# Kernel optimization log

Hardware: AMD Instinct MI355X
Metric: run time of the kernel (lower is better)

The kernel has to match this reference:

```python
import jax, jax.numpy as jnp
import numpy as np

KNOW, ITEM, D, L, LAT, B, S = 1024, 20000, 128, 2, 256, 256, 200
NTOT = ITEM + KNOW
E1, E2 = 32768, 160000


def graph_layer(h, W, a, src, dst, n):
    # GAT-style: gather src/dst, edge MLP, segment softmax over dst, weighted scatter-sum
    z = h @ W                                              # [N, D]
    e = jax.nn.leaky_relu((jnp.concatenate([z[src], z[dst]], axis=-1) @ a)[:, 0])  # [E]
    m = jax.ops.segment_max(e, dst, num_segments=n)
    m = jnp.where(jnp.isfinite(m), m, 0.0)                 # nodes with no in-edges
    w = jnp.exp(e - m[dst])                                # [E]
    den = jax.ops.segment_sum(w, dst, num_segments=n)      # [N]
    num = jax.ops.segment_sum(w[:, None] * z[src], dst, num_segments=n)  # [N, D]
    return jnp.where(den[:, None] > 0, num / jnp.maximum(den, 1e-12)[:, None], 0.0)


def setup_inputs() -> dict:
    key = jax.random.key(0)
    ks = jax.random.split(key, 32)
    p = lambda i, shp: jax.random.normal(ks[i], shp, dtype=jnp.float32) * 0.05
    inp = {
        'p_rec': jax.random.randint(ks[0], (B, S), 0, ITEM),
        'p_target': jax.random.randint(ks[1], (B,), 0, S),
        'a_rec': jax.random.randint(ks[2], (B, S), 0, 3),
        'kn_rec': jax.random.uniform(ks[3], (B, S, KNOW), dtype=jnp.float32),
        'kn_num': jnp.ones((B, S), dtype=jnp.float32),
        'src1': jax.random.randint(ks[4], (E1,), 0, KNOW),
        'dst1': jax.random.randint(ks[5], (E1,), 0, KNOW),
        'src2': jax.random.randint(ks[6], (E2,), 0, NTOT),
        'dst2': jax.random.randint(ks[7], (E2,), 0, NTOT),
        'src3': jax.random.randint(ks[8], (E2,), 0, NTOT),
        'dst3': jax.random.randint(ks[9], (E2,), 0, NTOT),
        'kn_table': p(10, (KNOW, D)),
        'exer_table': p(11, (ITEM, D)),
        'ans_table': p(12, (3, D)),
        'gW': p(13, (L, 3, D, D)),
        'gA': p(14, (L, 3, 2 * D, 1)),
        'raW1': p(15, (L, D, D)),
        'raB1': jnp.zeros((L, D), jnp.float32),
        'raW2': p(16, (L, D, 1)),
        'actW1': p(17, (3 * D, LAT)),
        'actB1': jnp.zeros((LAT,), jnp.float32),
        'actW2': p(18, (LAT, ITEM)),
        'actB2': jnp.zeros((ITEM,), jnp.float32),
        'vW1': p(19, (3, 3 * D, LAT)),
        'vB1': jnp.zeros((3, LAT), jnp.float32),
        'vW2': p(20, (3, LAT, 1)),
        'vB2': jnp.zeros((3, 1), jnp.float32),
    }
    return inp


def reference(p_rec, p_target, a_rec, kn_rec, kn_num, src1, dst1, src2, dst2, src3, dst3,
              kn_table, exer_table, ans_table, gW, gA, raW1, raB1, raW2,
              actW1, actB1, actW2, actB2, vW1, vB1, vW2, vB2):
    kn, ex = kn_table, exer_table
    for l in range(L):  # GraphEncoder: stacked Fusion blocks (distinct params)
        k_dir = graph_layer(kn, gW[l, 0], gA[l, 0], src1, dst1, KNOW)
        ek = jnp.concatenate([ex, kn], axis=0)             # [NTOT, D]
        kfe = graph_layer(ek, gW[l, 1], gA[l, 1], src2, dst2, NTOT)
        efk = graph_layer(ek, gW[l, 2], gA[l, 2], src3, dst3, NTOT)
        A_, B_ = k_dir, kfe[ITEM:]
        ra = lambda x: jnp.tanh(x @ raW1[l] + raB1[l]) @ raW2[l]  # [KNOW, 1]
        s = jax.nn.softmax(jnp.concatenate([ra(A_), ra(B_)], axis=1), axis=1)
        kn = s[:, :1] * A_ + s[:, 1:2] * B_
        ex = efk[:ITEM]
    # hidden_layer
    be = ex[p_rec]                                         # [B, S, D]
    ba = ans_table[a_rec]                                  # [B, S, D]
    bk = jnp.einsum('bsk,kd->bsd', kn_rec, kn) / kn_num[..., None]
    item = jnp.concatenate([be, ba, bk], axis=-1)          # [B, S, 3D]
    m = (jnp.arange(S)[None, :] < (p_target + 1)[:, None]).astype(item.dtype)
    h = (item * m[..., None]).sum(axis=1) / m.sum(axis=1, keepdims=True)  # [B, 3D]
    logits = jnp.tanh(h @ actW1 + actB1) @ actW2 + actB2   # [B, ITEM]
    vh = jnp.tanh(jnp.einsum('bd,kdl->kbl', h, vW1) + vB1[:, None, :])
    vals = jnp.einsum('kbl,klo->kbo', vh, vW2) + vB2[:, None, :]  # [3, B, 1]
    return logits, vals[0], vals[1], vals[2]
```

## Files before the change

### kernel.cpp

```cpp
#include <hip/hip_runtime.h>

#define D 128
#define KNOW 1024
#define ITEM 20000
#define NTOT (ITEM + KNOW)
#define LAYERS 2
#define LAT 256
#define BB 256
#define SS 200
#define H3 (3 * D)
#define CH 4
#define ZROWS 64
#define NBK (KNOW / ZROWS)
#define NBN ((NTOT + ZROWS - 1) / ZROWS)
#define NZT (NBK + 2 * NBN)
#define NAGGU (KNOW / 4 + ITEM / 4)
#define NKROW (BB * CH)
#define XPITCH 68
#define NLOGB ((ITEM + 255) / 256)
#define NLV (NLOGB * (BB / 32))
#define NVB ((3 * BB + 3) / 4)

__global__ __launch_bounds__(256) void zdv_ker(
    const float* __restrict__ Xe, const float* __restrict__ Xk,
    const float* __restrict__ gW, const float* __restrict__ gA, int layer,
    float* __restrict__ z1, float* __restrict__ z2, float* __restrict__ z3,
    float* __restrict__ ds1, float* __restrict__ dd1,
    float* __restrict__ ds2, float* __restrict__ dd2,
    float* __restrict__ ds3, float* __restrict__ dd3)
{
    __shared__ __align__(16) float xT[D * XPITCH];
    int bid = blockIdx.x;
    int g, row0, nmax;
    if (bid < NBK)            { g = 0; row0 = bid * ZROWS;                nmax = KNOW; }
    else if (bid < NBK + NBN) { g = 1; row0 = (bid - NBK) * ZROWS;        nmax = NTOT; }
    else                      { g = 2; row0 = (bid - NBK - NBN) * ZROWS;  nmax = NTOT; }
    const float* W = gW + (size_t)(layer * 3 + g) * D * D;
    const float* A = gA + (size_t)(layer * 3 + g) * 2 * D;
    float* Z  = (g == 0) ? z1  : (g == 1 ? z2  : z3);
    float* DS = (g == 0) ? ds1 : (g == 1 ? ds2 : ds3);
    float* DD = (g == 0) ? dd1 : (g == 1 ? dd2 : dd3);

    int tid = threadIdx.x;
#pragma unroll
    for (int i = 0; i < 8; ++i) {
        int flat = tid + i * 256;
        int row  = flat >> 5;
        int f4   = flat & 31;
        int grow = row0 + row;
        float4 v = make_float4(0.f, 0.f, 0.f, 0.f);
        if (grow < nmax) {
            const float* src = (g == 0) ? (Xk + (size_t)grow * D)
                             : (grow < ITEM ? Xe + (size_t)grow * D
                                            : Xk + (size_t)(grow - ITEM) * D);
            v = *(const float4*)(src + f4 * 4);
        }
        int slot = row ^ ((f4 & 7) << 2);
        int kk = f4 * 4;
        xT[(kk + 0) * XPITCH + slot] = v.x;
        xT[(kk + 1) * XPITCH + slot] = v.y;
        xT[(kk + 2) * XPITCH + slot] = v.z;
        xT[(kk + 3) * XPITCH + slot] = v.w;
    }
    __syncthreads();

    int cg_ = tid & 31;
    int rg = tid >> 5;
    int c0 = cg_ * 4;
    int r0a = rg * 8, r0b = rg * 8 + 4;

    float acc[8][4];
#pragma unroll
    for (int r = 0; r < 8; ++r)
#pragma unroll
        for (int c = 0; c < 4; ++c) acc[r][c] = 0.f;

#pragma unroll 4
    for (int k = 0; k < D; ++k) {
        float4 wv = *(const float4*)(W + (size_t)k * D + c0);
        int xc = ((k >> 2) & 7) << 2;
        float4 xa = *(const float4*)&xT[k * XPITCH + (r0a ^ xc)];
        float4 xb = *(const float4*)&xT[k * XPITCH + (r0b ^ xc)];
        acc[0][0] = fmaf(xa.x, wv.x, acc[0][0]); acc[0][1] = fmaf(xa.x, wv.y, acc[0][1]);
        acc[0][2] = fmaf(xa.x, wv.z, acc[0][2]); acc[0][3] = fmaf(xa.x, wv.w, acc[0][3]);
        acc[1][0] = fmaf(xa.y, wv.x, acc[1][0]); acc[1][1] = fmaf(xa.y, wv.y, acc[1][1]);
        acc[1][2] = fmaf(xa.y, wv.z, acc[1][2]); acc[1][3] = fmaf(xa.y, wv.w, acc[1][3]);
        acc[2][0] = fmaf(xa.z, wv.x, acc[2][0]); acc[2][1] = fmaf(xa.z, wv.y, acc[2][1]);
        acc[2][2] = fmaf(xa.z, wv.z, acc[2][2]); acc[2][3] = fmaf(xa.z, wv.w, acc[2][3]);
        acc[3][0] = fmaf(xa.w, wv.x, acc[3][0]); acc[3][1] = fmaf(xa.w, wv.y, acc[3][1]);
        acc[3][2] = fmaf(xa.w, wv.z, acc[3][2]); acc[3][3] = fmaf(xa.w, wv.w, acc[3][3]);
        acc[4][0] = fmaf(xb.x, wv.x, acc[4][0]); acc[4][1] = fmaf(xb.x, wv.y, acc[4][1]);
        acc[4][2] = fmaf(xb.x, wv.z, acc[4][2]); acc[4][3] = fmaf(xb.x, wv.w, acc[4][3]);
        acc[5][0] = fmaf(xb.y, wv.x, acc[5][0]); acc[5][1] = fmaf(xb.y, wv.y, acc[5][1]);
        acc[5][2] = fmaf(xb.y, wv.z, acc[5][2]); acc[5][3] = fmaf(xb.y, wv.w, acc[5][3]);
        acc[6][0] = fmaf(xb.z, wv.x, acc[6][0]); acc[6][1] = fmaf(xb.z, wv.y, acc[6][1]);
        acc[6][2] = fmaf(xb.z, wv.z, acc[6][2]); acc[6][3] = fmaf(xb.z, wv.w, acc[6][3]);
        acc[7][0] = fmaf(xb.w, wv.x, acc[7][0]); acc[7][1] = fmaf(xb.w, wv.y, acc[7][1]);
        acc[7][2] = fmaf(xb.w, wv.z, acc[7][2]); acc[7][3] = fmaf(xb.w, wv.w, acc[7][3]);
    }

#pragma unroll
    for (int r = 0; r < 8; ++r) {
        int grow = row0 + ((r < 4) ? (r0a + r) : (r0b + r - 4));
        if (grow < nmax) {
            float4 v = make_float4(acc[r][0], acc[r][1], acc[r][2], acc[r][3]);
            *(float4*)(Z + (size_t)grow * D + c0) = v;
        }
    }

    float4 as = *(const float4*)(A + c0);
    float4 ad = *(const float4*)(A + D + c0);
    float ps[8], pd[8];
#pragma unroll
    for (int r = 0; r < 8; ++r) {
        ps[r] = acc[r][0] * as.x + acc[r][1] * as.y + acc[r][2] * as.z + acc[r][3] * as.w;
        pd[r] = acc[r][0] * ad.x + acc[r][1] * ad.y + acc[r][2] * ad.z + acc[r][3] * ad.w;
    }
#pragma unroll
    for (int m = 16; m; m >>= 1) {
#pragma unroll
        for (int r = 0; r < 8; ++r) {
            ps[r] += __shfl_xor(ps[r], m, 64);
            pd[r] += __shfl_xor(pd[r], m, 64);
        }
    }
    if (cg_ == 0) {
#pragma unroll
        for (int r = 0; r < 8; ++r) {
            int grow = row0 + ((r < 4) ? (r0a + r) : (r0b + r - 4));
            if (grow < nmax) { DS[grow] = ps[r]; DD[grow] = pd[r]; }
        }
    }
}

__global__ void hist3(const int* __restrict__ d1, const int* __restrict__ d2, const int* __restrict__ d3,
                      int E1, int E2, int* __restrict__ c1, int* __restrict__ c2, int* __restrict__ c3) {
    int i = blockIdx.x * blockDim.x + threadIdx.x;
    if (i < E1) atomicAdd(&c1[d1[i]], 1);
    else if (i < E1 + E2) { int d = d2[i - E1]; if (d >= ITEM) atomicAdd(&c2[d - ITEM], 1); }
    else if (i < E1 + 2 * E2) { int d = d3[i - E1 - E2]; if (d < ITEM) atomicAdd(&c3[d], 1); }
}

__global__ __launch_bounds__(1024) void exscan3(int* __restrict__ c1, int* __restrict__ o1,
                                                int* __restrict__ c2, int* __restrict__ o2,
                                                int* __restrict__ c3, int* __restrict__ o3) {
    int g = blockIdx.x;
    int* cnt = (g == 0) ? c1 : (g == 1 ? c2 : c3);
    int* off = (g == 0) ? o1 : (g == 1 ? o2 : o3);
    int n = (g == 2) ? ITEM : KNOW;
    int tid = threadIdx.x, lane = tid & 63, wid = tid >> 6;
    int L = (n + 1023) >> 10;
    int i0 = tid * L;
    int sum = 0;
    for (int q = 0; q < L; ++q) {
        int i = i0 + q;
        if (i < n) sum += cnt[i];
    }
    int x = sum;
#pragma unroll
    for (int d = 1; d < 64; d <<= 1) { int t = __shfl_up(x, d, 64); if (lane >= d) x += t; }
    __shared__ int ws[16];
    if (lane == 63) ws[wid] = x;
    __syncthreads();
    if (wid == 0) {
        int w = (lane < 16) ? ws[lane] : 0;
#pragma unroll
        for (int d = 1; d < 16; d <<= 1) { int t = __shfl_up(w, d, 64); if (lane >= d) w += t; }
        if (lane < 16) ws[lane] = w;
    }
    __syncthreads();
    int run = x - sum + ((wid > 0) ? ws[wid - 1] : 0);
    if (tid == 0) off[0] = 0;
    for (int q = 0; q < L; ++q) {
        int i = i0 + q;
        if (i < n) {
            int v = cnt[i];
            cnt[i] = run;
            run += v;
            off[i + 1] = run;
        }
    }
}

__global__ void scatter3(const int* __restrict__ s1, const int* __restrict__ d1,
                         const int* __restrict__ s2, const int* __restrict__ d2,
                         const int* __restrict__ s3, const int* __restrict__ d3,
                         int E1, int E2, int* __restrict__ cur1, int* __restrict__ cur2, int* __restrict__ cur3,
                         int* __restrict__ e1, int* __restrict__ e2, int* __restrict__ e3) {
    int i = blockIdx.x * blockDim.x + threadIdx.x;
    if (i < E1) { int p = atomicAdd(&cur1[d1[i]], 1); e1[p] = s1[i]; }
    else if (i < E1 + E2) { int j = i - E1; int d = d2[j]; if (d >= ITEM) { int p = atomicAdd(&cur2[d - ITEM], 1); e2[p] = s2[j]; } }
    else if (i < E1 + 2 * E2) { int j = i - E1 - E2; int d = d3[j]; if (d < ITEM) { int p = atomicAdd(&cur3[d], 1); e3[p] = s3[j]; } }
}

__device__ __forceinline__ void agg_row(const float* __restrict__ Z, const float* __restrict__ dsrc,
                                        float dd, const int* __restrict__ es, int e0, int e1,
                                        int lane, float* __restrict__ acc) {
#pragma unroll
    for (int q = 0; q < 8; ++q) acc[q] = 0.f;
    if (e1 <= e0) return;
    float mx = -3.4e38f;
    for (int e = e0 + lane; e < e1; e += 64) {
        float t = dsrc[es[e]] + dd;
        t = (t > 0.f) ? t : 0.01f * t;
        mx = fmaxf(mx, t);
    }
#pragma unroll
    for (int o = 32; o; o >>= 1) mx = fmaxf(mx, __shfl_xor(mx, o, 64));
    int eg = lane >> 4, cs = lane & 15;
    float den = 0.f;
    for (int e = e0 + eg; e < e1; e += 4) {
        int s = es[e];
        float t = dsrc[s] + dd;
        t = (t > 0.f) ? t : 0.01f * t;
        float w = __expf(t - mx);
        den += w;
        const float4* zr = (const float4*)(Z + (size_t)s * D + cs * 8);
        float4 za = zr[0], zb = zr[1];
        acc[0] = fmaf(w, za.x, acc[0]); acc[1] = fmaf(w, za.y, acc[1]);
        acc[2] = fmaf(w, za.z, acc[2]); acc[3] = fmaf(w, za.w, acc[3]);
        acc[4] = fmaf(w, zb.x, acc[4]); acc[5] = fmaf(w, zb.y, acc[5]);
        acc[6] = fmaf(w, zb.z, acc[6]); acc[7] = fmaf(w, zb.w, acc[7]);
    }
#pragma unroll
    for (int m = 16; m <= 32; m <<= 1) {
        den += __shfl_xor(den, m, 64);
#pragma unroll
        for (int q = 0; q < 8; ++q) acc[q] += __shfl_xor(acc[q], m, 64);
    }
    float inv = 1.f / fmaxf(den, 1e-12f);
#pragma unroll
    for (int q = 0; q < 8; ++q) acc[q] *= inv;
}

__global__ __launch_bounds__(256) void agg3c(
    const float* __restrict__ z1, const float* __restrict__ z2, const float* __restrict__ z3,
    const float* __restrict__ ds1, const float* __restrict__ dd1,
    const float* __restrict__ ds2, const float* __restrict__ dd2,
    const float* __restrict__ ds3, const float* __restrict__ dd3,
    const int* __restrict__ off1, const int* __restrict__ es1,
    const int* __restrict__ off2, const int* __restrict__ es2,
    const int* __restrict__ off3, const int* __restrict__ es3,
    const float* __restrict__ raW1L, const float* __restrict__ raB1L,
    const float* __restrict__ raW2L, float* __restrict__ buf,
    const float* __restrict__ kn_rec, const float* __restrict__ kn_num,
    const int* __restrict__ p_target, float* __restrict__ krowP)
{
    int wv = threadIdx.x >> 6, lane = threadIdx.x & 63;
    int eg = lane >> 4, cs = lane & 15;
    int u = blockIdx.x;
    if (u < KNOW / 4) {
        __shared__ float ABs[4][2][D];
        int i = u * 4 + wv;
        float accA[8], accB[8];
        agg_row(z1, ds1, dd1[i], es1, off1[i], off1[i + 1], lane, accA);
        agg_row(z2, ds2, dd2[ITEM + i], es2, off2[i], off2[i + 1], lane, accB);
        if (eg == 0) {
            *(float4*)&ABs[wv][0][cs * 8]     = make_float4(accA[0], accA[1], accA[2], accA[3]);
            *(float4*)&ABs[wv][0][cs * 8 + 4] = make_float4(accA[4], accA[5], accA[6], accA[7]);
            *(float4*)&ABs[wv][1][cs * 8]     = make_float4(accB[0], accB[1], accB[2], accB[3]);
            *(float4*)&ABs[wv][1][cs * 8 + 4] = make_float4(accB[4], accB[5], accB[6], accB[7]);
        }
        __syncthreads();
        int j0 = lane * 2;
        float b0 = raB1L[j0], b1 = raB1L[j0 + 1];
        float aA0 = b0, aA1 = b1, aB0 = b0, aB1 = b1;
#pragma unroll 4
        for (int k = 0; k < D; ++k) {
            float av = ABs[wv][0][k], bv = ABs[wv][1][k];
            float2 w = *(const float2*)(raW1L + (size_t)k * D + j0);
            aA0 = fmaf(av, w.x, aA0); aA1 = fmaf(av, w.y, aA1);
            aB0 = fmaf(bv, w.x, aB0); aB1 = fmaf(bv, w.y, aB1);
        }
        float2 w2 = *(const float2*)(raW2L + j0);
        float pA = tanhf(aA0) * w2.x + tanhf(aA1) * w2.y;
        float pB = tanhf(aB0) * w2.x + tanhf(aB1) * w2.y;
#pragma unroll
        for (int o = 32; o; o >>= 1) { pA += __shfl_xor(pA, o, 64); pB += __shfl_xor(pB, o, 64); }
        float mx2 = fmaxf(pA, pB);
        float eA = __expf(pA - mx2), eB = __expf(pB - mx2);
        float s = 1.f / (eA + eB);
        float sA = eA * s, sB = eB * s;
        float2 Av = *(float2*)&ABs[wv][0][j0];
        float2 Bv = *(float2*)&ABs[wv][1][j0];
        *(float2*)(buf + (size_t)(ITEM + i) * D + j0) =
            make_float2(sA * Av.x + sB * Bv.x, sA * Av.y + sB * Bv.y);
    } else if (u < NAGGU) {
        int row = (u - KNOW / 4) * 4 + wv;
        if (row < ITEM) {
            float acc[8];
            agg_row(z3, ds3, dd3[row], es3, off3[row], off3[row + 1], lane, acc);
            if (eg == 0) {
                *(float4*)(buf + (size_t)row * D + cs * 8)     = make_float4(acc[0], acc[1], acc[2], acc[3]);
                *(float4*)(buf + (size_t)row * D + cs * 8 + 4) = make_float4(acc[4], acc[5], acc[6], acc[7]);
            }
        }
    } else {
        int uk = u - NAGGU;
        int b = uk & (BB - 1), ch = uk >> 8;
        int cnt = p_target[b] + 1;
        int per = (SS + CH - 1) / CH;
        int s0 = ch * per, s1 = s0 + per;
        if (s1 > cnt) s1 = cnt;
        int k0 = threadIdx.x * 4;
        float4 a = make_float4(0.f, 0.f, 0.f, 0.f);
        for (int s = s0; s < s1; ++s) {
            float inv = 1.f / kn_num[b * SS + s];
            float4 v = *(const float4*)(kn_rec + ((size_t)b * SS + s) * KNOW + k0);
            a.x += v.x * inv; a.y += v.y * inv; a.z += v.z * inv; a.w += v.w * inv;
        }
        *(float4*)(krowP + ((size_t)ch * BB + b) * KNOW + k0) = a;
    }
}

__global__ __launch_bounds__(512) void hker(const float* __restrict__ ex, const float* __restrict__ ans_table,
                                            const int* __restrict__ p_rec, const int* __restrict__ a_rec,
                                            const int* __restrict__ p_target, const float* __restrict__ krowP,
                                            const float* __restrict__ kn, float* __restrict__ h) {
    int b = blockIdx.x;
    int j = threadIdx.x & 127, sg = threadIdx.x >> 7;
    int cnt = p_target[b] + 1;
    __shared__ int pidx[SS], aidx[SS];
    __shared__ float kr[KNOW];
    __shared__ float red[4][3][128];
    for (int i = threadIdx.x; i < cnt; i += 512) { pidx[i] = p_rec[b * SS + i]; aidx[i] = a_rec[b * SS + i]; }
    for (int i = threadIdx.x; i < KNOW; i += 512) {
        float s = 0.f;
#pragma unroll
        for (int c = 0; c < CH; ++c) s += krowP[((size_t)c * BB + b) * KNOW + i];
        kr[i] = s;
    }
    __syncthreads();
    float accE = 0.f, accA = 0.f;
    for (int s = sg; s < cnt; s += 4) {
        accE += ex[(size_t)pidx[s] * D + j];
        accA += ans_table[aidx[s] * D + j];
    }
    float accK = 0.f;
    for (int k = sg * 256; k < sg * 256 + 256; ++k) accK += kr[k] * kn[(size_t)k * D + j];
    red[sg][0][j] = accE; red[sg][1][j] = accA; red[sg][2][j] = accK;
    __syncthreads();
    if (sg == 0) {
        float inv = 1.f / (float)cnt;
        float e = (red[0][0][j] + red[1][0][j] + red[2][0][j] + red[3][0][j]) * inv;
        float a = (red[0][1][j] + red[1][1][j] + red[2][1][j] + red[3][1][j]) * inv;
        float kv = (red[0][2][j] + red[1][2][j] + red[2][2][j] + red[3][2][j]) * inv;
        h[b * H3 + j] = e;
        h[b * H3 + D + j] = a;
        h[b * H3 + 2 * D + j] = kv;
    }
}

__global__ __launch_bounds__(256) void hidden_gemm(const float* __restrict__ h,
                                                   const float* __restrict__ actW1, const float* __restrict__ actB1,
                                                   const float* __restrict__ vW1, const float* __restrict__ vB1,
                                                   float* __restrict__ hid) {
    __shared__ float hT[H3 * 17];
    int tid = threadIdx.x;
    int b0 = blockIdx.y * 16;
    for (int idx = tid; idx < 16 * H3; idx += 256) {
        int r = idx / H3, k = idx - r * H3;
        hT[k * 17 + r] = h[(size_t)(b0 + r) * H3 + k];
    }
    __syncthreads();
    int j = blockIdx.x * 64 + (tid & 63);
    int head = j >> 8, jj = j & 255;
    int rg = tid >> 6, r0 = rg * 4;
    const float* W = (head == 0) ? actW1 : (vW1 + (size_t)(head - 1) * H3 * LAT);
    float bias = (head == 0) ? actB1[jj] : vB1[(head - 1) * LAT + jj];
    float acc[4] = {bias, bias, bias, bias};
#pragma unroll 4
    for (int k = 0; k < H3; ++k) {
        float w = W[(size_t)k * LAT + jj];
        float h0 = hT[k * 17 + r0 + 0];
        float h1 = hT[k * 17 + r0 + 1];
        float h2 = hT[k * 17 + r0 + 2];
        float h3 = hT[k * 17 + r0 + 3];
        acc[0] = fmaf(h0, w, acc[0]);
        acc[1] = fmaf(h1, w, acc[1]);
        acc[2] = fmaf(h2, w, acc[2]);
        acc[3] = fmaf(h3, w, acc[3]);
    }
#pragma unroll
    for (int r = 0; r < 4; ++r)
        hid[((size_t)head * BB + (b0 + r0 + r)) * LAT + jj] = tanhf(acc[r]);
}

__global__ __launch_bounds__(256) void logitsvals(const float* __restrict__ hid,
                                                  const float* __restrict__ actW2, const float* __restrict__ actB2,
                                                  const float* __restrict__ vW2, const float* __restrict__ vB2,
                                                  float* __restrict__ out) {
    int bid = blockIdx.x;
    int tid = threadIdx.x;
    if (bid < NLV) {
        __shared__ float hT[LAT * 33];
        int ix = bid % NLOGB, iy = bid / NLOGB;
        int b0 = iy * 32;
        for (int idx = tid; idx < 32 * LAT; idx += 256) {
            int r = idx >> 8, k = idx & 255;
            hT[k * 33 + r] = hid[(size_t)(b0 + r) * LAT + k];
        }
        __syncthreads();
        int lane6 = tid & 63;
        int rg = tid >> 6, r0 = rg * 8;
        int ibase = ix * 256 + lane6;
        int icol[4], icl[4];
        float bias[4];
#pragma unroll
        for (int c = 0; c < 4; ++c) {
            icol[c] = ibase + c * 64;
            icl[c] = icol[c] < ITEM ? icol[c] : (ITEM - 1);
            bias[c] = actB2[icl[c]];
        }
        float acc[8][4];
#pragma unroll
        for (int r = 0; r < 8; ++r)
#pragma unroll
            for (int c = 0; c < 4; ++c) acc[r][c] = bias[c];
#pragma unroll 2
        for (int k = 0; k < LAT; ++k) {
            float w0 = actW2[(size_t)k * ITEM + icl[0]];
            float w1 = actW2[(size_t)k * ITEM + icl[1]];
            float w2 = actW2[(size_t)k * ITEM + icl[2]];
            float w3 = actW2[(size_t)k * ITEM + icl[3]];
            const float* hp = &hT[k * 33 + r0];
#pragma unroll
            for (int r = 0; r < 8; ++r) {
                float hv = hp[r];
                acc[r][0] = fmaf(hv, w0, acc[r][0]);
                acc[r][1] = fmaf(hv, w1, acc[r][1]);
                acc[r][2] = fmaf(hv, w2, acc[r][2]);
                acc[r][3] = fmaf(hv, w3, acc[r][3]);
            }
        }
#pragma unroll
        for (int c = 0; c < 4; ++c) {
            if (icol[c] < ITEM) {
#pragma unroll
                for (int r = 0; r < 8; ++r)
                    out[(size_t)(b0 + r0 + r) * ITEM + icol[c]] = acc[r][c];
            }
        }
    } else {
        int idx = (bid - NLV) * 4 + (tid >> 6);
        int lane = tid & 63;
        if (idx >= 3 * BB) return;
        int k = idx / BB, b = idx - k * BB;
        const float* vh = hid + ((size_t)(k + 1) * BB + b) * LAT;
        float4 a = ((const float4*)vh)[lane];
        float4 w = ((const float4*)(vW2 + k * LAT))[lane];
        float s = a.x * w.x + a.y * w.y + a.z * w.z + a.w * w.w;
#pragma unroll
        for (int o = 32; o; o >>= 1) s += __shfl_down(s, o, 64);
        if (lane == 0) out[(size_t)BB * ITEM + k * BB + b] = s + vB2[k];
    }
}

extern "C" void kernel_launch(void* const* d_in, const int* in_sizes, int n_in,
                              void* d_out, int out_size, void* d_ws, size_t ws_size,
                              hipStream_t stream) {
    const int*   p_rec      = (const int*)d_in[0];
    const int*   p_target   = (const int*)d_in[1];
    const int*   a_rec      = (const int*)d_in[2];
    const float* kn_rec     = (const float*)d_in[3];
    const float* kn_num     = (const float*)d_in[4];
    const int*   src1       = (const int*)d_in[5];
    const int*   dst1       = (const int*)d_in[6];
    const int*   src2       = (const int*)d_in[7];
    const int*   dst2       = (const int*)d_in[8];
    const int*   src3       = (const int*)d_in[9];
    const int*   dst3       = (const int*)d_in[10];
    const float* kn_table   = (const float*)d_in[11];
    const float* exer_table = (const float*)d_in[12];
    const float* ans_table  = (const float*)d_in[13];
    const float* gW         = (const float*)d_in[14];
    const float* gA         = (const float*)d_in[15];
    const float* raW1       = (const float*)d_in[16];
    const float* raB1       = (const float*)d_in[17];
    const float* raW2       = (const float*)d_in[18];
    const float* actW1      = (const float*)d_in[19];
    const float* actB1      = (const float*)d_in[20];
    const float* actW2      = (const float*)d_in[21];
    const float* actB2      = (const float*)d_in[22];
    const float* vW1        = (const float*)d_in[23];
    const float* vB1        = (const float*)d_in[24];
    const float* vW2        = (const float*)d_in[25];
    const float* vB2        = (const float*)d_in[26];
    const int E1 = in_sizes[5], E2 = in_sizes[7];

    float* base = (float*)d_ws;
    size_t o = 0;
    auto alloc = [&](size_t n) -> float* { float* p = base + o; o += (n + 3) & ~(size_t)3; return p; };
    float* buf  = alloc((size_t)NTOT * D);
    float* z1   = alloc((size_t)KNOW * D);
    float* z2   = alloc((size_t)NTOT * D);
    float* z3   = alloc((size_t)NTOT * D);
    float* ds1 = alloc(KNOW);  float* dd1 = alloc(KNOW);
    float* ds2 = alloc(NTOT);  float* dd2 = alloc(NTOT);
    float* ds3 = alloc(NTOT);  float* dd3 = alloc(NTOT);
    int* cnts = (int*)alloc(2 * KNOW + NTOT);
    int* cnt1 = cnts, *cnt2 = cnts + KNOW, *cnt3 = cnts + 2 * KNOW;
    int* off1 = (int*)alloc(KNOW + 1);
    int* off2 = (int*)alloc(KNOW + 1);
    int* off3 = (int*)alloc(ITEM + 1);
    int* es1  = (int*)alloc(E1);
    int* es2  = (int*)alloc(E2);
    int* es3  = (int*)alloc(E2);
    float* krowP = alloc((size_t)CH * BB * KNOW);
    float* hbuf  = alloc((size_t)BB * H3);
    float* hid   = alloc((size_t)4 * BB * LAT);

    hipMemsetAsync(cnts, 0, sizeof(int) * (2 * KNOW + NTOT), stream);

    int etot = E1 + 2 * E2;
    hist3<<<(etot + 255) / 256, 256, 0, stream>>>(dst1, dst2, dst3, E1, E2, cnt1, cnt2, cnt3);
    exscan3<<<3, 1024, 0, stream>>>(cnt1, off1, cnt2, off2, cnt3, off3);
    scatter3<<<(etot + 255) / 256, 256, 0, stream>>>(src1, dst1, src2, dst2, src3, dst3,
                                                     E1, E2, cnt1, cnt2, cnt3, es1, es2, es3);

    for (int l = 0; l < LAYERS; ++l) {
        const float* Xe = (l == 0) ? exer_table : buf;
        const float* Xk = (l == 0) ? kn_table : (buf + (size_t)ITEM * D);
        zdv_ker<<<NZT, 256, 0, stream>>>(Xe, Xk, gW, gA, l, z1, z2, z3,
                                         ds1, dd1, ds2, dd2, ds3, dd3);
        int nb = NAGGU + ((l == 0) ? NKROW : 0);
        agg3c<<<nb, 256, 0, stream>>>(z1, z2, z3, ds1, dd1, ds2, dd2, ds3, dd3,
                                      off1, es1, off2, es2, off3, es3,
                                      raW1 + (size_t)l * D * D, raB1 + (size_t)l * D,
                                      raW2 + (size_t)l * D, buf,
                                      kn_rec, kn_num, p_target, krowP);
    }

    hker<<<BB, 512, 0, stream>>>(buf, ans_table, p_rec, a_rec, p_target, krowP, buf + (size_t)ITEM * D, hbuf);
    hidden_gemm<<<dim3(16, 16), 256, 0, stream>>>(hbuf, actW1, actB1, vW1, vB1, hid);
    logitsvals<<<NLV + NVB, 256, 0, stream>>>(hid, actW2, actB2, vW2, vB2, (float*)d_out);
}
```

Baseline: 303.5 us.

## Fold graph-2 projection past aggregation and drop softmax max pass

Graph 2 only needs outputs for the KNOW target nodes. Its full-NTOT z=h@W is removed: the attention logits use a precomputed W·a vector applied to the raw inputs, the raw X rows are aggregated, and W is multiplied in afterwards for only the 1024 knowledge rows. Input and output buffers are double-buffered because agg3c now reads the previous layer's X. The segment-max pass in the softmax is also removed and exp is applied to unshifted logits, which saves a full edge sweep but risks overflow for large logits.

```diff
diff --git a/kernel.cpp b/kernel.cpp
--- a/kernel.cpp
+++ b/kernel.cpp
@@ -13,7 +13,7 @@
 #define ZROWS 64
 #define NBK (KNOW / ZROWS)
 #define NBN ((NTOT + ZROWS - 1) / ZROWS)
-#define NZT (NBK + 2 * NBN)
+#define NZT (NBK + NBN)
 #define NAGGU (KNOW / 4 + ITEM / 4)
 #define NKROW (BB * CH)
 #define XPITCH 68
@@ -23,8 +23,9 @@
 
 __global__ __launch_bounds__(256) void zdv_ker(
     const float* __restrict__ Xe, const float* __restrict__ Xk,
-    const float* __restrict__ gW, const float* __restrict__ gA, int layer,
-    float* __restrict__ z1, float* __restrict__ z2, float* __restrict__ z3,
+    const float* __restrict__ gW, const float* __restrict__ gA,
+    const float* __restrict__ wa2, int layer,
+    float* __restrict__ z1, float* __restrict__ z3,
     float* __restrict__ ds1, float* __restrict__ dd1,
     float* __restrict__ ds2, float* __restrict__ dd2,
     float* __restrict__ ds3, float* __restrict__ dd3)
@@ -32,14 +33,13 @@
     __shared__ __align__(16) float xT[D * XPITCH];
     int bid = blockIdx.x;
     int g, row0, nmax;
-    if (bid < NBK)            { g = 0; row0 = bid * ZROWS;                nmax = KNOW; }
-    else if (bid < NBK + NBN) { g = 1; row0 = (bid - NBK) * ZROWS;        nmax = NTOT; }
-    else                      { g = 2; row0 = (bid - NBK - NBN) * ZROWS;  nmax = NTOT; }
+    if (bid < NBK) { g = 0; row0 = bid * ZROWS;          nmax = KNOW; }
+    else           { g = 2; row0 = (bid - NBK) * ZROWS;  nmax = NTOT; }
     const float* W = gW + (size_t)(layer * 3 + g) * D * D;
     const float* A = gA + (size_t)(layer * 3 + g) * 2 * D;
-    float* Z  = (g == 0) ? z1  : (g == 1 ? z2  : z3);
-    float* DS = (g == 0) ? ds1 : (g == 1 ? ds2 : ds3);
-    float* DD = (g == 0) ? dd1 : (g == 1 ? dd2 : dd3);
+    float* Z  = (g == 0) ? z1  : z3;
+    float* DS = (g == 0) ? ds1 : ds3;
+    float* DD = (g == 0) ? dd1 : dd3;
 
     int tid = threadIdx.x;
 #pragma unroll
@@ -131,6 +131,40 @@
             if (grow < nmax) { DS[grow] = ps[r]; DD[grow] = pd[r]; }
         }
     }
+
+    if (g == 2) {
+        const float* was = wa2 + (size_t)layer * 2 * D;
+        float4 ws4 = *(const float4*)(was + c0);
+        float4 wd4 = *(const float4*)(was + D + c0);
+        int xc = ((c0 >> 2) & 7) << 2;
+        float pxs[8], pxd[8];
+#pragma unroll
+        for (int r = 0; r < 8; ++r) {
+            int rr = (r < 4) ? (r0a + r) : (r0b + r - 4);
+            int sl = rr ^ xc;
+            float x0 = xT[(c0 + 0) * XPITCH + sl];
+            float x1 = xT[(c0 + 1) * XPITCH + sl];
+            float x2 = xT[(c0 + 2) * XPITCH + sl];
+            float x3 = xT[(c0 + 3) * XPITCH + sl];
+            pxs[r] = x0 * ws4.x + x1 * ws4.y + x2 * ws4.z + x3 * ws4.w;
+            pxd[r] = x0 * wd4.x + x1 * wd4.y + x2 * wd4.z + x3 * wd4.w;
+        }
+#pragma unroll
+        for (int m = 16; m; m >>= 1) {
+#pragma unroll
+            for (int r = 0; r < 8; ++r) {
+                pxs[r] += __shfl_xor(pxs[r], m, 64);
+                pxd[r] += __shfl_xor(pxd[r], m, 64);
+            }
+        }
+        if (cg_ == 0) {
+#pragma unroll
+            for (int r = 0; r < 8; ++r) {
+                int grow = row0 + ((r < 4) ? (r0a + r) : (r0b + r - 4));
+                if (grow < nmax) { ds2[grow] = pxs[r]; dd2[grow] = pxd[r]; }
+            }
+        }
+    }
 }
 
 __global__ void hist3(const int* __restrict__ d1, const int* __restrict__ d2, const int* __restrict__ d3,
@@ -143,8 +177,24 @@
 
 __global__ __launch_bounds__(1024) void exscan3(int* __restrict__ c1, int* __restrict__ o1,
                                                 int* __restrict__ c2, int* __restrict__ o2,
-                                                int* __restrict__ c3, int* __restrict__ o3) {
+                                                int* __restrict__ c3, int* __restrict__ o3,
+                                                const float* __restrict__ gW, const float* __restrict__ gA,
+                                                float* __restrict__ wa2) {
     int g = blockIdx.x;
+    if (g == 3) {
+        int t = threadIdx.x;
+        if (t < 2 * 2 * D) {
+            int l = t >> 8, rem = t & 255;
+            int v = rem >> 7, k = rem & 127;
+            const float* Wp = gW + (size_t)(l * 3 + 1) * D * D + (size_t)k * D;
+            const float* ap = gA + (size_t)(l * 3 + 1) * 2 * D + v * D;
+            float s = 0.f;
+#pragma unroll 4
+            for (int j = 0; j < D; ++j) s = fmaf(Wp[j], ap[j], s);
+            wa2[(l * 2 + v) * D + k] = s;
+        }
+        return;
+    }
     int* cnt = (g == 0) ? c1 : (g == 1 ? c2 : c3);
     int* off = (g == 0) ? o1 : (g == 1 ? o2 : o3);
     int n = (g == 2) ? ITEM : KNOW;
@@ -199,21 +249,14 @@
 #pragma unroll
     for (int q = 0; q < 8; ++q) acc[q] = 0.f;
     if (e1 <= e0) return;
-    float mx = -3.4e38f;
-    for (int e = e0 + lane; e < e1; e += 64) {
-        float t = dsrc[es[e]] + dd;
-        t = (t > 0.f) ? t : 0.01f * t;
-        mx = fmaxf(mx, t);
-    }
-#pragma unroll
-    for (int o = 32; o; o >>= 1) mx = fmaxf(mx, __shfl_xor(mx, o, 64));
     int eg = lane >> 4, cs = lane & 15;
     float den = 0.f;
+#pragma unroll 2
     for (int e = e0 + eg; e < e1; e += 4) {
         int s = es[e];
         float t = dsrc[s] + dd;
         t = (t > 0.f) ? t : 0.01f * t;
-        float w = __expf(t - mx);
+        float w = __expf(t);
         den += w;
         const float4* zr = (const float4*)(Z + (size_t)s * D + cs * 8);
         float4 za = zr[0], zb = zr[1];
@@ -233,16 +276,53 @@
     for (int q = 0; q < 8; ++q) acc[q] *= inv;
 }
 
+__device__ __forceinline__ void agg_rowX(const float* __restrict__ Xe, const float* __restrict__ Xk,
+                                         const float* __restrict__ dsrc, float dd,
+                                         const int* __restrict__ es, int e0, int e1,
+                                         int lane, float* __restrict__ acc) {
+#pragma unroll
+    for (int q = 0; q < 8; ++q) acc[q] = 0.f;
+    if (e1 <= e0) return;
+    int eg = lane >> 4, cs = lane & 15;
+    float den = 0.f;
+#pragma unroll 2
+    for (int e = e0 + eg; e < e1; e += 4) {
+        int s = es[e];
+        float t = dsrc[s] + dd;
+        t = (t > 0.f) ? t : 0.01f * t;
+        float w = __expf(t);
+        den += w;
+        const float* xr = (s < ITEM) ? (Xe + (size_t)s * D) : (Xk + (size_t)(s - ITEM) * D);
+        const float4* zr = (const float4*)(xr + cs * 8);
+        float4 za = zr[0], zb = zr[1];
+        acc[0] = fmaf(w, za.x, acc[0]); acc[1] = fmaf(w, za.y, acc[1]);
+        acc[2] = fmaf(w, za.z, acc[2]); acc[3] = fmaf(w, za.w, acc[3]);
+        acc[4] = fmaf(w, zb.x, acc[4]); acc[5] = fmaf(w, zb.y, acc[5]);
+        acc[6] = fmaf(w, zb.z, acc[6]); acc[7] = fmaf(w, zb.w, acc[7]);
+    }
+#pragma unroll
+    for (int m = 16; m <= 32; m <<= 1) {
+        den += __shfl_xor(den, m, 64);
+#pragma unroll
+        for (int q = 0; q < 8; ++q) acc[q] += __shfl_xor(acc[q], m, 64);
+    }
+    float inv = 1.f / fmaxf(den, 1e-12f);
+#pragma unroll
+    for (int q = 0; q < 8; ++q) acc[q] *= inv;
+}
+
 __global__ __launch_bounds__(256) void agg3c(
-    const float* __restrict__ z1, const float* __restrict__ z2, const float* __restrict__ z3,
+    const float* __restrict__ Xe, const float* __restrict__ Xk,
+    const float* __restrict__ z1, const float* __restrict__ z3,
     const float* __restrict__ ds1, const float* __restrict__ dd1,
     const float* __restrict__ ds2, const float* __restrict__ dd2,
     const float* __restrict__ ds3, const float* __restrict__ dd3,
     const int* __restrict__ off1, const int* __restrict__ es1,
     const int* __restrict__ off2, const int* __restrict__ es2,
     const int* __restrict__ off3, const int* __restrict__ es3,
+    const float* __restrict__ gW1L,
     const float* __restrict__ raW1L, const float* __restrict__ raB1L,
-    const float* __restrict__ raW2L, float* __restrict__ buf,
+    const float* __restrict__ raW2L, float* __restrict__ out,
     const float* __restrict__ kn_rec, const float* __restrict__ kn_num,
     const int* __restrict__ p_target, float* __restrict__ krowP)
 {
@@ -251,10 +331,11 @@
     int u = blockIdx.x;
     if (u < KNOW / 4) {
         __shared__ float ABs[4][2][D];
+        __shared__ float Bf[4][D];
         int i = u * 4 + wv;
         float accA[8], accB[8];
         agg_row(z1, ds1, dd1[i], es1, off1[i], off1[i + 1], lane, accA);
-        agg_row(z2, ds2, dd2[ITEM + i], es2, off2[i], off2[i + 1], lane, accB);
+        agg_rowX(Xe, Xk, ds2, dd2[ITEM + i], es2, off2[i], off2[i + 1], lane, accB);
         if (eg == 0) {
             *(float4*)&ABs[wv][0][cs * 8]     = make_float4(accA[0], accA[1], accA[2], accA[3]);
             *(float4*)&ABs[wv][0][cs * 8 + 4] = make_float4(accA[4], accA[5], accA[6], accA[7]);
@@ -263,11 +344,20 @@
         }
         __syncthreads();
         int j0 = lane * 2;
+        float fB0 = 0.f, fB1 = 0.f;
+#pragma unroll 4
+        for (int k = 0; k < D; ++k) {
+            float xv = ABs[wv][1][k];
+            float2 w = *(const float2*)(gW1L + (size_t)k * D + j0);
+            fB0 = fmaf(xv, w.x, fB0); fB1 = fmaf(xv, w.y, fB1);
+        }
+        Bf[wv][j0] = fB0; Bf[wv][j0 + 1] = fB1;
+        __syncthreads();
         float b0 = raB1L[j0], b1 = raB1L[j0 + 1];
         float aA0 = b0, aA1 = b1, aB0 = b0, aB1 = b1;
 #pragma unroll 4
         for (int k = 0; k < D; ++k) {
-            float av = ABs[wv][0][k], bv = ABs[wv][1][k];
+            float av = ABs[wv][0][k], bv = Bf[wv][k];
             float2 w = *(const float2*)(raW1L + (size_t)k * D + j0);
             aA0 = fmaf(av, w.x, aA0); aA1 = fmaf(av, w.y, aA1);
             aB0 = fmaf(bv, w.x, aB0); aB1 = fmaf(bv, w.y, aB1);
@@ -282,8 +372,8 @@
         float s = 1.f / (eA + eB);
         float sA = eA * s, sB = eB * s;
         float2 Av = *(float2*)&ABs[wv][0][j0];
-        float2 Bv = *(float2*)&ABs[wv][1][j0];
-        *(float2*)(buf + (size_t)(ITEM + i) * D + j0) =
+        float2 Bv = make_float2(Bf[wv][j0], Bf[wv][j0 + 1]);
+        *(float2*)(out + (size_t)(ITEM + i) * D + j0) =
             make_float2(sA * Av.x + sB * Bv.x, sA * Av.y + sB * Bv.y);
     } else if (u < NAGGU) {
         int row = (u - KNOW / 4) * 4 + wv;
@@ -291,8 +381,8 @@
             float acc[8];
             agg_row(z3, ds3, dd3[row], es3, off3[row], off3[row + 1], lane, acc);
             if (eg == 0) {
-                *(float4*)(buf + (size_t)row * D + cs * 8)     = make_float4(acc[0], acc[1], acc[2], acc[3]);
-                *(float4*)(buf + (size_t)row * D + cs * 8 + 4) = make_float4(acc[4], acc[5], acc[6], acc[7]);
+                *(float4*)(out + (size_t)row * D + cs * 8)     = make_float4(acc[0], acc[1], acc[2], acc[3]);
+                *(float4*)(out + (size_t)row * D + cs * 8 + 4) = make_float4(acc[4], acc[5], acc[6], acc[7]);
             }
         }
     } else {
@@ -491,13 +581,14 @@
     float* base = (float*)d_ws;
     size_t o = 0;
     auto alloc = [&](size_t n) -> float* { float* p = base + o; o += (n + 3) & ~(size_t)3; return p; };
-    float* buf  = alloc((size_t)NTOT * D);
+    float* buf0 = alloc((size_t)NTOT * D);
+    float* buf1 = alloc((size_t)NTOT * D);
     float* z1   = alloc((size_t)KNOW * D);
-    float* z2   = alloc((size_t)NTOT * D);
     float* z3   = alloc((size_t)NTOT * D);
     float* ds1 = alloc(KNOW);  float* dd1 = alloc(KNOW);
     float* ds2 = alloc(NTOT);  float* dd2 = alloc(NTOT);
     float* ds3 = alloc(NTOT);  float* dd3 = alloc(NTOT);
+    float* wa2 = alloc(2 * 2 * D);
     int* cnts = (int*)alloc(2 * KNOW + NTOT);
     int* cnt1 = cnts, *cnt2 = cnts + KNOW, *cnt3 = cnts + 2 * KNOW;
     int* off1 = (int*)alloc(KNOW + 1);
@@ -514,24 +605,26 @@
 
     int etot = E1 + 2 * E2;
     hist3<<<(etot + 255) / 256, 256, 0, stream>>>(dst1, dst2, dst3, E1, E2, cnt1, cnt2, cnt3);
-    exscan3<<<3, 1024, 0, stream>>>(cnt1, off1, cnt2, off2, cnt3, off3);
+    exscan3<<<4, 1024, 0, stream>>>(cnt1, off1, cnt2, off2, cnt3, off3, gW, gA, wa2);
     scatter3<<<(etot + 255) / 256, 256, 0, stream>>>(src1, dst1, src2, dst2, src3, dst3,
                                                      E1, E2, cnt1, cnt2, cnt3, es1, es2, es3);
 
     for (int l = 0; l < LAYERS; ++l) {
-        const float* Xe = (l == 0) ? exer_table : buf;
-        const float* Xk = (l == 0) ? kn_table : (buf + (size_t)ITEM * D);
-        zdv_ker<<<NZT, 256, 0, stream>>>(Xe, Xk, gW, gA, l, z1, z2, z3,
+        const float* Xe = (l == 0) ? exer_table : buf0;
+        const float* Xk = (l == 0) ? kn_table : (buf0 + (size_t)ITEM * D);
+        float* out = (l == 0) ? buf0 : buf1;
+        zdv_ker<<<NZT, 256, 0, stream>>>(Xe, Xk, gW, gA, wa2, l, z1, z3,
                                          ds1, dd1, ds2, dd2, ds3, dd3);
         int nb = NAGGU + ((l == 0) ? NKROW : 0);
-        agg3c<<<nb, 256, 0, stream>>>(z1, z2, z3, ds1, dd1, ds2, dd2, ds3, dd3,
+        agg3c<<<nb, 256, 0, stream>>>(Xe, Xk, z1, z3, ds1, dd1, ds2, dd2, ds3, dd3,
                                       off1, es1, off2, es2, off3, es3,
+                                      gW + (size_t)(l * 3 + 1) * D * D,
                                       raW1 + (size_t)l * D * D, raB1 + (size_t)l * D,
-                                      raW2 + (size_t)l * D, buf,
+                                      raW2 + (size_t)l * D, out,
                                       kn_rec, kn_num, p_target, krowP);
     }
 
-    hker<<<BB, 512, 0, stream>>>(buf, ans_table, p_rec, a_rec, p_target, krowP, buf + (size_t)ITEM * D, hbuf);
+    hker<<<BB, 512, 0, stream>>>(buf1, ans_table, p_rec, a_rec, p_target, krowP, buf1 + (size_t)ITEM * D, hbuf);
     hidden_gemm<<<dim3(16, 16), 256, 0, stream>>>(hbuf, actW1, actB1, vW1, vB1, hid);
     logitsvals<<<NLV + NVB, 256, 0, stream>>>(hid, actW2, actB2, vW2, vB2, (float*)d_out);
 }
```

After: 299.9 us. About the same (-1.2%).
